# Performance work log

Hardware: AMD Instinct MI355X
Metric: run time of the kernel (lower is better)

Reference implementation:

```python
import jax, jax.numpy as jnp
import numpy as np

N, E = 50000, 1600000
IN_DIM, OUT_DIM = 256, 256


def setup_inputs() -> dict:
    key = jax.random.key(0)
    ks = jax.random.split(key, 9)
    def xavier(k, shape):
        fan_in, fan_out = shape[1], shape[0]
        a = jnp.sqrt(6.0 / (fan_in + fan_out))
        return jax.random.uniform(k, shape, jnp.float32, -a, a)
    return {
        "x": jax.random.normal(ks[0], (N, IN_DIM), jnp.float32),
        "edge_index": jax.random.randint(ks[1], (2, E), 0, N, jnp.int64 if jax.config.jax_enable_x64 else jnp.int32),
        "edge_attr": jax.random.uniform(ks[2], (E,), jnp.float32),
        # GCNConv linear (no bias inside lin; bias added after aggregation)
        "W_gcn": xavier(ks[3], (OUT_DIM, IN_DIM)),
        "b_gcn": jnp.zeros((OUT_DIM,), jnp.float32),
        # MLP: Linear(in+out -> out), tanh, Linear(out -> out), tanh
        "W1": xavier(ks[4], (OUT_DIM, IN_DIM + OUT_DIM)),
        "b1": jnp.zeros((OUT_DIM,), jnp.float32),
        "W2": xavier(ks[5], (OUT_DIM, OUT_DIM)),
        "b2": jnp.zeros((OUT_DIM,), jnp.float32),
    }


def gcn_conv(x, edge_index, W, b):
    n = x.shape[0]
    # add self loops
    loops = jnp.arange(n, dtype=edge_index.dtype)
    row = jnp.concatenate([edge_index[0], loops])  # source
    col = jnp.concatenate([edge_index[1], loops])  # target
    # symmetric normalization with edge_weight = 1
    deg = jax.ops.segment_sum(jnp.ones_like(col, dtype=x.dtype), col, num_segments=n)
    dinv = jnp.where(deg > 0, jax.lax.rsqrt(deg), 0.0)
    norm = dinv[row] * dinv[col]  # [E+N]
    xw = x @ W.T  # [N, out_dim]
    msgs = xw[row] * norm[:, None]  # gather + scale
    out = jax.ops.segment_sum(msgs, col, num_segments=n)  # scatter-add
    return out + b


def reference(x, edge_index, edge_attr, W_gcn, b_gcn, W1, b1, W2, b2):
    # edge_attr is accepted but unused by the original module's routing
    x1 = jnp.tanh(gcn_conv(x, edge_index, W_gcn, b_gcn))
    h = jnp.concatenate([x, x1], axis=1)  # [N, in+out]
    h = jnp.tanh(h @ W1.T + b1)
    return jnp.tanh(h @ W2.T + b2)
```

## Files before the change

### kernel.cpp

```cpp
#include <hip/hip_runtime.h>
#include <stdint.h>

typedef __attribute__((ext_vector_type(8))) short bf16x8_t;
typedef __attribute__((ext_vector_type(4))) float f32x4_t;

#define GLOAD_LDS16(gp, lp) __builtin_amdgcn_global_load_lds( \
    (__attribute__((address_space(1))) void*)(void*)(gp),      \
    (__attribute__((address_space(3))) void*)(lp), 16, 0, 0)

#define CSR_STRIDE 96

__device__ __forceinline__ float bf2f(unsigned short u) {
  union { unsigned int i; float f; } c; c.i = ((unsigned int)u) << 16; return c.f;
}
__device__ __forceinline__ unsigned short f2bf(float f) {
  unsigned int x = __float_as_uint(f);
  unsigned int r = (x + 0x7fffu + ((x >> 16) & 1u)) >> 16;
  return (unsigned short)r;
}
__device__ __forceinline__ float fast_tanh(float x) {
  const float cx = fminf(fmaxf(x, -15.f), 15.f);
  const float e  = __expf(2.f * cx);
  return __fdividef(e - 1.f, e + 1.f);
}

__global__ void prep_kernel(const float* __restrict__ x, unsigned short* __restrict__ xh,
                            const float* __restrict__ Wg, const float* __restrict__ W1,
                            const float* __restrict__ W2, unsigned short* __restrict__ Wg_b,
                            unsigned short* __restrict__ W1_b, unsigned short* __restrict__ W2_b,
                            int* __restrict__ cursor, unsigned short* __restrict__ xws,
                            int n, int total) {
  const int gid = blockIdx.x * blockDim.x + threadIdx.x;
  const int i = gid * 4;
  if (i < total) {
    float4 v = *(const float4*)(x + i);
    int row = i >> 8, col = i & 255;
    ushort4 o;
    o.x = f2bf(v.x); o.y = f2bf(v.y); o.z = f2bf(v.z); o.w = f2bf(v.w);
    *(ushort4*)(xh + (size_t)row * 512 + col) = o;
  }
  if (gid < n) cursor[gid] = 0;
  if (gid < 256) xws[((size_t)(gid >> 5) * (n + 1) + n) * 32 + (gid & 31)] = 0;
  if (gid < 65536) {
    const float* src; unsigned short* dst; int off;
    if (i < 65536)              { src = Wg; dst = Wg_b; off = i; }
    else if (i < 65536 + 131072){ src = W1; dst = W1_b; off = i - 65536; }
    else                        { src = W2; dst = W2_b; off = i - (65536 + 131072); }
    float4 v = *(const float4*)(src + off);
    ushort4 o;
    o.x = f2bf(v.x); o.y = f2bf(v.y); o.z = f2bf(v.z); o.w = f2bf(v.w);
    *(ushort4*)(dst + off) = o;
  }
}

__global__ void fill_kernel(const int* __restrict__ esrc, const int* __restrict__ edst,
                            int* __restrict__ cursor, unsigned short* __restrict__ csr16, int E) {
  int i = blockIdx.x * blockDim.x + threadIdx.x;
  if (i < E) {
    int d = edst[i];
    int pos = atomicAdd(&cursor[d], 1);
    if (pos < CSR_STRIDE) csr16[(size_t)d * CSR_STRIDE + pos] = (unsigned short)esrc[i];
  }
}

__global__ __launch_bounds__(256)
void agg_kernel(const unsigned short* __restrict__ xws, const unsigned short* __restrict__ csr16,
                const int* __restrict__ cursor, const float* __restrict__ bias,
                unsigned short* __restrict__ xh, int n) {
  const int tid   = threadIdx.x;
  const int wid   = tid >> 6;
  const int lane  = tid & 63;
  const int slice = blockIdx.x & 7;
  const int node  = (blockIdx.x >> 3) * 4 + wid;
  if (node >= n) return;
  const int g   = lane >> 3;
  const int gl4 = (lane & 7) * 4;
  const unsigned short* sbase = xws + (size_t)slice * (n + 1) * 32 + gl4;
  const int ZROW = n;

  float a0 = 0.f, a1 = 0.f, a2 = 0.f, a3 = 0.f;
  const int cnt = cursor[node];
  const unsigned short* crow = csr16 + (size_t)node * CSR_STRIDE;
  for (int base = 0; base <= cnt; base += 64) {
    const int il = base + lane;
    int pv = (int)crow[il];
    pv = (il == cnt) ? node : pv;
    const int rem = cnt - base;
#pragma unroll
    for (int b = 0; b < 8; ++b) {
      const int idx = b * 8 + g;
      const int sv  = __builtin_amdgcn_ds_bpermute(idx << 2, pv);
      const int src = (idx <= rem) ? sv : ZROW;
      const ushort4 v = *(const ushort4*)(sbase + ((unsigned)src << 5));
      a0 += bf2f(v.x); a1 += bf2f(v.y); a2 += bf2f(v.z); a3 += bf2f(v.w);
    }
  }
#pragma unroll
  for (int mask = 8; mask < 64; mask <<= 1) {
    a0 += __shfl_xor(a0, mask);
    a1 += __shfl_xor(a1, mask);
    a2 += __shfl_xor(a2, mask);
    a3 += __shfl_xor(a3, mask);
  }
  if (lane < 8) {
    const float di = rsqrtf((float)(cnt + 1));
    const int c0 = slice * 32 + gl4;
    ushort4 o;
    o.x = f2bf(fast_tanh(a0 * di + bias[c0 + 0]));
    o.y = f2bf(fast_tanh(a1 * di + bias[c0 + 1]));
    o.z = f2bf(fast_tanh(a2 * di + bias[c0 + 2]));
    o.w = f2bf(fast_tanh(a3 * di + bias[c0 + 3]));
    *(ushort4*)(xh + (size_t)node * 512 + 256 + c0) = o;
  }
}

__global__ __launch_bounds__(256, 2)
void gemm1_kernel(const unsigned short* __restrict__ A, int lda,
                  const unsigned short* __restrict__ B,
                  const int* __restrict__ degc,
                  unsigned short* __restrict__ Cp, int M, int K) {
  __shared__ __align__(16) unsigned short As[128 * 64];
  __shared__ __align__(16) unsigned short Bs[128 * 64];
  const int tid  = threadIdx.x;
  const int lane = tid & 63;
  const int wid  = tid >> 6;
  const int wm = wid & 1, wn = wid >> 1;
  const int tileM = blockIdx.x * 128;
  const int tileN = blockIdx.y * 128;

  const int rowInCh = lane >> 3;
  const int slot    = lane & 7;
  const int srcOff  = ((slot ^ rowInCh) * 8);

  f32x4_t acc[4][4];
#pragma unroll
  for (int m = 0; m < 4; ++m)
#pragma unroll
    for (int n = 0; n < 4; ++n) acc[m][n] = (f32x4_t){0.f, 0.f, 0.f, 0.f};

  for (int kt = 0; kt < K; kt += 64) {
#pragma unroll
    for (int cc = 0; cc < 4; ++cc) {
      const int c = wid * 4 + cc;
      const int r = c * 8 + rowInCh;
      const int rA = min(tileM + r, M - 1);
      GLOAD_LDS16(A + (size_t)rA * lda + (kt + srcOff), As + c * 512 + lane * 8);
      GLOAD_LDS16(B + (size_t)(tileN + r) * K + (kt + srcOff), Bs + c * 512 + lane * 8);
    }
    __syncthreads();
#pragma unroll
    for (int ks = 0; ks < 2; ++ks) {
      bf16x8_t af[4], bfr[4];
      const int ksl = ks * 4 + (lane >> 4);
#pragma unroll
      for (int m = 0; m < 4; ++m) {
        const int ra = wm * 64 + m * 16 + (lane & 15);
        af[m]  = *(const bf16x8_t*)(As + ra * 64 + ((ksl ^ (ra & 7)) * 8));
        const int rb = wn * 64 + m * 16 + (lane & 15);
        bfr[m] = *(const bf16x8_t*)(Bs + rb * 64 + ((ksl ^ (rb & 7)) * 8));
      }
#pragma unroll
      for (int m = 0; m < 4; ++m)
#pragma unroll
        for (int n = 0; n < 4; ++n)
          acc[m][n] = __builtin_amdgcn_mfma_f32_16x16x32_bf16(af[m], bfr[n], acc[m][n], 0, 0, 0);
    }
    __syncthreads();
  }

  const int colBase = tileN + wn * 64 + (lane & 15);
  const int rowBase = tileM + wm * 64 + ((lane >> 4) << 2);
#pragma unroll
  for (int m = 0; m < 4; ++m) {
    const int gr0 = rowBase + m * 16;
#pragma unroll
    for (int r = 0; r < 4; ++r) {
      const int gr = gr0 + r;
      if (gr < M) {
        const float rs = rsqrtf((float)(degc[gr] + 1));
#pragma unroll
        for (int n = 0; n < 4; ++n) {
          const int gc = colBase + n * 16;
          Cp[((size_t)(gc >> 5) * (M + 1) + gr) * 32 + (gc & 31)] = f2bf(acc[m][n][r] * rs);
        }
      }
    }
  }
}

template<bool TANH, int OUT_MODE>
__global__ __launch_bounds__(256, 2)
void gemm_bt_kernel(const unsigned short* __restrict__ A, int lda,
                    const unsigned short* __restrict__ B,
                    const float* __restrict__ bias,
                    void* __restrict__ Cp, int ldc, int M, int K) {
  __shared__ __align__(16) unsigned short As[128 * 64];
  __shared__ __align__(16) unsigned short Bs[128 * 64];
  const int tid  = threadIdx.x;
  const int lane = tid & 63;
  const int wid  = tid >> 6;
  const int wm = wid & 1, wn = wid >> 1;
  const int tileM = blockIdx.x * 128;
  const int tileN = blockIdx.y * 128;

  const int rowInCh = lane >> 3;
  const int slot    = lane & 7;
  const int srcOff  = ((slot ^ rowInCh) * 8);

  f32x4_t acc[4][4];
#pragma unroll
  for (int m = 0; m < 4; ++m)
#pragma unroll
    for (int n = 0; n < 4; ++n) acc[m][n] = (f32x4_t){0.f, 0.f, 0.f, 0.f};

  for (int kt = 0; kt < K; kt += 64) {
#pragma unroll
    for (int cc = 0; cc < 4; ++cc) {
      const int c = wid * 4 + cc;
      const int r = c * 8 + rowInCh;
      const int rA = min(tileM + r, M - 1);
      GLOAD_LDS16(A + (size_t)rA * lda + (kt + srcOff), As + c * 512 + lane * 8);
      GLOAD_LDS16(B + (size_t)(tileN + r) * K + (kt + srcOff), Bs + c * 512 + lane * 8);
    }
    __syncthreads();
#pragma unroll
    for (int ks = 0; ks < 2; ++ks) {
      bf16x8_t af[4], bfr[4];
      const int ksl = ks * 4 + (lane >> 4);
#pragma unroll
      for (int m = 0; m < 4; ++m) {
        const int ra = wm * 64 + m * 16 + (lane & 15);
        af[m]  = *(const bf16x8_t*)(As + ra * 64 + ((ksl ^ (ra & 7)) * 8));
        const int rb = wn * 64 + m * 16 + (lane & 15);
        bfr[m] = *(const bf16x8_t*)(Bs + rb * 64 + ((ksl ^ (rb & 7)) * 8));
      }
#pragma unroll
      for (int m = 0; m < 4; ++m)
#pragma unroll
        for (int n = 0; n < 4; ++n)
          acc[m][n] = __builtin_amdgcn_mfma_f32_16x16x32_bf16(af[m], bfr[n], acc[m][n], 0, 0, 0);
    }
    __syncthreads();
  }

  const int colBase = tileN + wn * 64 + (lane & 15);
  const int rowBase = tileM + wm * 64 + ((lane >> 4) << 2);
#pragma unroll
  for (int n = 0; n < 4; ++n) {
    const int gc = colBase + n * 16;
    const float bv = bias[gc];
#pragma unroll
    for (int m = 0; m < 4; ++m) {
      const int gr0 = rowBase + m * 16;
#pragma unroll
      for (int r = 0; r < 4; ++r) {
        const int gr = gr0 + r;
        if (gr < M) {
          float v = acc[m][n][r] + bv;
          if (TANH) v = fast_tanh(v);
          if (OUT_MODE == 0) ((float*)Cp)[(size_t)gr * ldc + gc] = v;
          else               ((unsigned short*)Cp)[(size_t)gr * ldc + gc] = f2bf(v);
        }
      }
    }
  }
}

extern "C" void kernel_launch(void* const* d_in, const int* in_sizes, int n_in,
                              void* d_out, int out_size, void* d_ws, size_t ws_size,
                              hipStream_t stream) {
  const float* x  = (const float*)d_in[0];
  const int*   ei = (const int*)d_in[1];
  const float* Wg = (const float*)d_in[3];
  const float* bg = (const float*)d_in[4];
  const float* W1 = (const float*)d_in[5];
  const float* b1 = (const float*)d_in[6];
  const float* W2 = (const float*)d_in[7];
  const float* b2 = (const float*)d_in[8];
  float* out = (float*)d_out;

  const int N = in_sizes[0] / 256;
  const int E = in_sizes[1] / 2;
  const int* esrc = ei;
  const int* edst = ei + E;

  unsigned short* xh = (unsigned short*)d_out;

  uint8_t* p = (uint8_t*)d_ws;
  auto alloc = [&](size_t bytes) { uint8_t* q = p; p += (bytes + 255) & ~(size_t)255; return q; };
  unsigned short* xws   = (unsigned short*)alloc((size_t)8 * (N + 1) * 32 * 2);
  unsigned short* h2    = (unsigned short*)alloc((size_t)N * 256 * 2);
  unsigned short* Wg_b  = (unsigned short*)alloc(256 * 256 * 2);
  unsigned short* W1_b  = (unsigned short*)alloc(256 * 512 * 2);
  unsigned short* W2_b  = (unsigned short*)alloc(256 * 256 * 2);
  int*            cursor= (int*)alloc((size_t)N * 4);
  unsigned short* csr16 = (unsigned short*)alloc(((size_t)N * CSR_STRIDE + 64) * 2);
  (void)ws_size; (void)n_in;

  prep_kernel<<<(N * 256 / 4 + 255) / 256, 256, 0, stream>>>(
      x, xh, Wg, W1, W2, Wg_b, W1_b, W2_b, cursor, xws, N, N * 256);
  fill_kernel<<<(E + 255) / 256, 256, 0, stream>>>(esrc, edst, cursor, csr16, E);

  dim3 gemm_grid((N + 127) / 128, 2);
  gemm1_kernel<<<gemm_grid, 256, 0, stream>>>(xh, 512, Wg_b, cursor, xws, N, 256);
  agg_kernel<<<8 * ((N + 3) / 4), 256, 0, stream>>>(xws, csr16, cursor, bg, xh, N);
  gemm_bt_kernel<true, 1><<<gemm_grid, 256, 0, stream>>>(xh, 512, W1_b, b1, h2, 256, N, 512);
  gemm_bt_kernel<true, 0><<<gemm_grid, 256, 0, stream>>>(h2, 256, W2_b, b2, out, 256, N, 256);
}
```

Before: 351.6 us.

## Remap GEMM blocks per XCD, raise occupancy, and process two edges per thread in fill

The GEMM launches become 1D grids with a block-to-tile mapping. Each XCD (blockIdx mod 8) gets a contiguous range of M tiles, and the two N tiles of the same M tile land on the same XCD, so A rows should be reused in that XCD's L2. Launch bounds go from 2 to 3 blocks per SM to allow more occupancy, which may force register spills. The CSR fill kernel now handles two edges per thread with int2 loads, which assumes E is even and 8-byte aligned.

```diff
diff --git a/kernel.cpp b/kernel.cpp
--- a/kernel.cpp
+++ b/kernel.cpp
@@ -22,6 +22,14 @@
   const float cx = fminf(fmaxf(x, -15.f), 15.f);
   const float e  = __expf(2.f * cx);
   return __fdividef(e - 1.f, e + 1.f);
+}
+
+__device__ __forceinline__ bool pair_map(int b, int mtPad8, int MT, int& m, int& n) {
+  const int xcd = b & 7;
+  const int idx = b >> 4;
+  n = (b >> 3) & 1;
+  m = xcd * mtPad8 + idx;
+  return m < MT;
 }
 
 __global__ void prep_kernel(const float* __restrict__ x, unsigned short* __restrict__ xh,
@@ -55,11 +63,16 @@
 
 __global__ void fill_kernel(const int* __restrict__ esrc, const int* __restrict__ edst,
                             int* __restrict__ cursor, unsigned short* __restrict__ csr16, int E) {
-  int i = blockIdx.x * blockDim.x + threadIdx.x;
+  int i = (blockIdx.x * blockDim.x + threadIdx.x) * 2;
   if (i < E) {
-    int d = edst[i];
-    int pos = atomicAdd(&cursor[d], 1);
-    if (pos < CSR_STRIDE) csr16[(size_t)d * CSR_STRIDE + pos] = (unsigned short)esrc[i];
+    const int2 s = *(const int2*)(esrc + i);
+    const int2 d = *(const int2*)(edst + i);
+    int pos0 = atomicAdd(&cursor[d.x], 1);
+    if (pos0 < CSR_STRIDE) csr16[(size_t)d.x * CSR_STRIDE + pos0] = (unsigned short)s.x;
+    if (i + 1 < E) {
+      int pos1 = atomicAdd(&cursor[d.y], 1);
+      if (pos1 < CSR_STRIDE) csr16[(size_t)d.y * CSR_STRIDE + pos1] = (unsigned short)s.y;
+    }
   }
 }
 
@@ -114,19 +127,21 @@
   }
 }
 
-__global__ __launch_bounds__(256, 2)
+__global__ __launch_bounds__(256, 3)
 void gemm1_kernel(const unsigned short* __restrict__ A, int lda,
                   const unsigned short* __restrict__ B,
                   const int* __restrict__ degc,
-                  unsigned short* __restrict__ Cp, int M, int K) {
+                  unsigned short* __restrict__ Cp, int M, int K, int mtPad8) {
   __shared__ __align__(16) unsigned short As[128 * 64];
   __shared__ __align__(16) unsigned short Bs[128 * 64];
+  int mi, ni;
+  if (!pair_map(blockIdx.x, mtPad8, (M + 127) / 128, mi, ni)) return;
   const int tid  = threadIdx.x;
   const int lane = tid & 63;
   const int wid  = tid >> 6;
   const int wm = wid & 1, wn = wid >> 1;
-  const int tileM = blockIdx.x * 128;
-  const int tileN = blockIdx.y * 128;
+  const int tileM = mi * 128;
+  const int tileN = ni * 128;
 
   const int rowInCh = lane >> 3;
   const int slot    = lane & 7;
@@ -189,19 +204,21 @@
 }
 
 template<bool TANH, int OUT_MODE>
-__global__ __launch_bounds__(256, 2)
+__global__ __launch_bounds__(256, 3)
 void gemm_bt_kernel(const unsigned short* __restrict__ A, int lda,
                     const unsigned short* __restrict__ B,
                     const float* __restrict__ bias,
-                    void* __restrict__ Cp, int ldc, int M, int K) {
+                    void* __restrict__ Cp, int ldc, int M, int K, int mtPad8) {
   __shared__ __align__(16) unsigned short As[128 * 64];
   __shared__ __align__(16) unsigned short Bs[128 * 64];
+  int mi, ni;
+  if (!pair_map(blockIdx.x, mtPad8, (M + 127) / 128, mi, ni)) return;
   const int tid  = threadIdx.x;
   const int lane = tid & 63;
   const int wid  = tid >> 6;
   const int wm = wid & 1, wn = wid >> 1;
-  const int tileM = blockIdx.x * 128;
-  const int tileN = blockIdx.y * 128;
+  const int tileM = mi * 128;
+  const int tileN = ni * 128;
 
   const int rowInCh = lane >> 3;
   const int slot    = lane & 7;
@@ -299,11 +316,13 @@
 
   prep_kernel<<<(N * 256 / 4 + 255) / 256, 256, 0, stream>>>(
       x, xh, Wg, W1, W2, Wg_b, W1_b, W2_b, cursor, xws, N, N * 256);
-  fill_kernel<<<(E + 255) / 256, 256, 0, stream>>>(esrc, edst, cursor, csr16, E);
-
-  dim3 gemm_grid((N + 127) / 128, 2);
-  gemm1_kernel<<<gemm_grid, 256, 0, stream>>>(xh, 512, Wg_b, cursor, xws, N, 256);
+  fill_kernel<<<(E / 2 + 255) / 256, 256, 0, stream>>>(esrc, edst, cursor, csr16, E);
+
+  const int MT = (N + 127) / 128;
+  const int mtPad8 = (MT + 7) / 8;
+  const int gemm_grid = mtPad8 * 8 * 2;
+  gemm1_kernel<<<gemm_grid, 256, 0, stream>>>(xh, 512, Wg_b, cursor, xws, N, 256, mtPad8);
   agg_kernel<<<8 * ((N + 3) / 4), 256, 0, stream>>>(xws, csr16, cursor, bg, xh, N);
-  gemm_bt_kernel<true, 1><<<gemm_grid, 256, 0, stream>>>(xh, 512, W1_b, b1, h2, 256, N, 512);
-  gemm_bt_kernel<true, 0><<<gemm_grid, 256, 0, stream>>>(h2, 256, W2_b, b2, out, 256, N, 256);
-}
+  gemm_bt_kernel<true, 1><<<gemm_grid, 256, 0, stream>>>(xh, 512, W1_b, b1, h2, 256, N, 512, mtPad8);
+  gemm_bt_kernel<true, 0><<<gemm_grid, 256, 0, stream>>>(h2, 256, W2_b, b2, out, 256, N, 256, mtPad8);
+}
```

New measurement: 359.6 us. 2.3% more time.
